# Optimization experiments

Hardware: AMD Instinct MI355X
Metric: run time of the kernel (lower is better)

Reference implementation:

```python
import jax, jax.numpy as jnp
import numpy as np

EMBED_DIM = 1024
NUM_HEADS = 16
NUM_GROUPS = 4
HEAD_DIM = EMBED_DIM // NUM_HEADS          # 64
KV_REPEAT = NUM_HEADS // NUM_GROUPS        # 4
KV_DIM = HEAD_DIM * NUM_GROUPS             # 256


def setup_inputs() -> dict:
    key = jax.random.key(0)
    ks = jax.random.split(key, 9)
    s = 0.02
    x = jax.random.normal(ks[0], (4, 2048, EMBED_DIM), dtype=jnp.float32)
    Wq = jax.random.normal(ks[1], (EMBED_DIM, EMBED_DIM), dtype=jnp.float32) * s
    bq = jnp.zeros((EMBED_DIM,), dtype=jnp.float32)
    Wk = jax.random.normal(ks[2], (EMBED_DIM, KV_DIM), dtype=jnp.float32) * s
    bk = jnp.zeros((KV_DIM,), dtype=jnp.float32)
    Wv = jax.random.normal(ks[3], (EMBED_DIM, KV_DIM), dtype=jnp.float32) * s
    bv = jnp.zeros((KV_DIM,), dtype=jnp.float32)
    Wo = jax.random.normal(ks[4], (EMBED_DIM, EMBED_DIM), dtype=jnp.float32) * s
    bo = jnp.zeros((EMBED_DIM,), dtype=jnp.float32)
    return {"x": x, "Wq": Wq, "bq": bq, "Wk": Wk, "bk": bk,
            "Wv": Wv, "bv": bv, "Wo": Wo, "bo": bo}


def reference(x, Wq, bq, Wk, bk, Wv, bv, Wo, bo):
    B, S, E = x.shape
    G, R, D = NUM_GROUPS, KV_REPEAT, HEAD_DIM
    scale = 1.0 / jnp.sqrt(jnp.float32(D))
    # projections
    q = (x @ Wq + bq).reshape(B, S, G, R, D)   # query head h = g*R + r, matching
    k = (x @ Wk + bk).reshape(B, S, G, D)      # torch repeat_interleave grouping
    v = (x @ Wv + bv).reshape(B, S, G, D)
    # scaled scores: [B, G, R, Sq, Sk] -- same O(n^2) math, no KV duplication
    scores = jnp.einsum('bqgrd,bkgd->bgrqk', q * scale, k)
    attn = jax.nn.softmax(scores, axis=-1)
    out = jnp.einsum('bgrqk,bkgd->bqgrd', attn, v).reshape(B, S, E)
    return out @ Wo + bo
```

## Files before the change

kernel.cpp:

```cpp
#include <hip/hip_runtime.h>
#include <hip/hip_bf16.h>
#include <cstdint>


#define B_  4
#define S_  2048
#define E_  1024
#define H_  16
#define G_  4
#define R_  4
#define D_  64
#define KV_ 256

typedef unsigned short u16;
typedef unsigned int u32;
typedef __attribute__((ext_vector_type(8))) __bf16 bf16x8;
typedef __attribute__((ext_vector_type(4))) float f32x4;

#if __has_builtin(__builtin_amdgcn_exp2f)
#define EXP2(x) __builtin_amdgcn_exp2f(x)
#else
#define EXP2(x) exp2f(x)
#endif

__device__ __forceinline__ float b2f(u16 v) {
    unsigned u = ((unsigned)v) << 16;
    return __builtin_bit_cast(float, u);
}
__device__ __forceinline__ u16 f2b(float f) {
    unsigned u = __builtin_bit_cast(unsigned, f);
    u += 0x7fffu + ((u >> 16) & 1u);
    return (u16)(u >> 16);
}
__device__ __forceinline__ u16 f2b_rtz(float f) {
    return (u16)(__builtin_bit_cast(unsigned, f) >> 16);
}

__device__ __forceinline__ int sniff_f32(const u16* w, int t) {
    bool hit = (w[t & 63] & 0x4000) != 0;
    return (__popcll(__ballot(hit)) > 4) ? 1 : 0;
}

__device__ __forceinline__ void gl_lds16(const u16* g, u16* l) {
    __builtin_amdgcn_global_load_lds(
        (const __attribute__((address_space(1))) u32*)(const void*)g,
        (__attribute__((address_space(3))) u32*)(void*)l, 16, 0, 0);
}

__global__ __launch_bounds__(256) void prep_all(
    const void* __restrict__ x,
    const void* __restrict__ Wq, const void* __restrict__ Wk,
    const void* __restrict__ Wv, const void* __restrict__ Wo,
    u16* __restrict__ xc, u16* __restrict__ WqT, u16* __restrict__ WkT,
    u16* __restrict__ WvT, u16* __restrict__ WoT)
{
    __shared__ u16 tile[64][65];
    const int f = sniff_f32((const u16*)Wq, threadIdx.x);
    int b = blockIdx.x;
    if (b < 4096) {
        int i0 = (b * 256 + threadIdx.x) * 8;
        if (f) {
            const float4* s = (const float4*)x;
            float4 a = s[i0 / 4], c = s[i0 / 4 + 1];
            uint4 o;
            o.x = (u32)f2b(a.x) | ((u32)f2b(a.y) << 16);
            o.y = (u32)f2b(a.z) | ((u32)f2b(a.w) << 16);
            o.z = (u32)f2b(c.x) | ((u32)f2b(c.y) << 16);
            o.w = (u32)f2b(c.z) | ((u32)f2b(c.w) << 16);
            *(uint4*)(xc + i0) = o;
        } else {
            *(uint4*)(xc + i0) = ((const uint4*)x)[i0 / 8];
        }
        return;
    }
    int j = b - 4096;
    const void* src; u16* dst; int N, nt, kt;
    if (j < 256)      {           src = Wq; dst = WqT; N = 1024; nt = j & 15; kt = j >> 4; }
    else if (j < 320) { j -= 256; src = Wk; dst = WkT; N = 256;  nt = j & 3;  kt = j >> 2; }
    else if (j < 384) { j -= 320; src = Wv; dst = WvT; N = 256;  nt = j & 3;  kt = j >> 2; }
    else              { j -= 384; src = Wo; dst = WoT; N = 1024; nt = j & 15; kt = j >> 4; }
    const int K = 1024;
    const int n0 = nt * 64, k0 = kt * 64;
    const int tr = threadIdx.x >> 6, tc = threadIdx.x & 63;
#pragma unroll
    for (int i = 0; i < 16; i++) {
        int k = k0 + i * 4 + tr;
        size_t idx = (size_t)k * N + n0 + tc;
        float v = f ? ((const float*)src)[idx] : b2f(((const u16*)src)[idx]);
        tile[i * 4 + tr][tc] = f2b(v);
    }
    __syncthreads();
#pragma unroll
    for (int i = 0; i < 16; i++) {
        int n = n0 + i * 4 + tr;
        dst[(size_t)n * K + k0 + tc] = tile[tc][i * 4 + tr];
    }
}

__device__ __forceinline__ float load_bias(const void* b, int i, int f) {
    return f ? ((const float*)b)[i] : b2f(((const u16*)b)[i]);
}

__global__ __launch_bounds__(256) void gemm_bt(
    const u16* __restrict__ A, const u16* __restrict__ Bt,
    const void* __restrict__ bA, const void* __restrict__ bB,
    const void* __restrict__ bC,
    void* __restrict__ Cv, void* __restrict__ Cv2, void* __restrict__ Cv3,
    int M, int N, int K, int mode, const u16* __restrict__ sniffw)
{
    __shared__ __align__(16) u16 As[128][64];
    __shared__ __align__(16) u16 Bs[128][64];

    const int t    = threadIdx.x;
    const int wave = t >> 6, lane = t & 63;
    const int lr   = lane & 15, quad = lane >> 4;
    const int kgrp = quad * 8;
    const int m0 = blockIdx.y * 128, n0 = blockIdx.x * 128;
    const int wm = (wave >> 1) * 64, wn = (wave & 1) * 64;
    const int f = sniff_f32(sniffw, t);

    f32x4 acc[4][4];
#pragma unroll
    for (int i = 0; i < 4; i++)
#pragma unroll
        for (int j = 0; j < 4; j++) acc[i][j] = (f32x4){0.f, 0.f, 0.f, 0.f};

    for (int k0 = 0; k0 < K; k0 += 64) {
#pragma unroll
        for (int i = 0; i < 4; i++) {
            int c = t + i * 256;
            int row = c >> 3, cc = (c & 7) * 8;
            int lbase = (i * 256 + wave * 64) * 8;
            gl_lds16(A  + (size_t)(m0 + row) * K + k0 + cc, &As[0][0] + lbase);
            gl_lds16(Bt + (size_t)(n0 + row) * K + k0 + cc, &Bs[0][0] + lbase);
        }
        __syncthreads();
#pragma unroll
        for (int s2 = 0; s2 < 2; ++s2) {
            bf16x8 af[4], bfr[4];
#pragma unroll
            for (int tm = 0; tm < 4; tm++)
                af[tm] = *(const bf16x8*)&As[wm + tm * 16 + lr][s2 * 32 + kgrp];
#pragma unroll
            for (int tn = 0; tn < 4; tn++)
                bfr[tn] = *(const bf16x8*)&Bs[wn + tn * 16 + lr][s2 * 32 + kgrp];
#pragma unroll
            for (int tm = 0; tm < 4; tm++)
#pragma unroll
                for (int tn = 0; tn < 4; tn++)
                    acc[tm][tn] = __builtin_amdgcn_mfma_f32_16x16x32_bf16(
                        af[tm], bfr[tn], acc[tm][tn], 0, 0, 0);
        }
        __syncthreads();
    }

#pragma unroll
    for (int tm = 0; tm < 4; tm++) {
        int rowb = m0 + wm + tm * 16 + quad * 4;
#pragma unroll
        for (int tn = 0; tn < 4; tn++) {
            int col = n0 + wn + tn * 16 + lr;
            float bv;
            if (mode == 2)           bv = load_bias(bA, col, f);
            else if (col < 1024)     bv = load_bias(bA, col, f);
            else if (col < 1280)     bv = load_bias(bB, col - 1024, f);
            else                     bv = load_bias(bC, col - 1280, f);
            if (mode == 4 && col >= 1280) {
                int c2 = col - 1280, g = c2 >> 6, d = c2 & 63;
                int bi = rowb >> 11, s = rowb & 2047;
                u16 h[4];
#pragma unroll
                for (int r = 0; r < 4; r++) h[r] = f2b(acc[tm][tn][r] + bv);
                uint2 pk;
                pk.x = (u32)h[0] | ((u32)h[1] << 16);
                pk.y = (u32)h[2] | ((u32)h[3] << 16);
                *(uint2*)&((u16*)Cv3)[((size_t)(bi * G_ + g) * D_ + d) * S_ + s] = pk;
                continue;
            }
#pragma unroll
            for (int r = 0; r < 4; r++) {
                int row = rowb + r;
                float val = acc[tm][tn][r] + bv;
                if (mode == 2) {
                    if (f) ((float*)Cv)[(size_t)row * N + col] = val;
                    else   ((u16*)Cv)[(size_t)row * N + col] = f2b(val);
                } else if (col < 1024) {
                    ((u16*)Cv)[(size_t)row * 1024 + col] = f2b(val * 0.18033688f);
                } else {
                    ((u16*)Cv2)[(size_t)row * 256 + (col - 1024)] = f2b(val);
                }
            }
        }
    }
}

__global__ __launch_bounds__(256) void flash_gqa(
    const u16* __restrict__ Q, const u16* __restrict__ Kb,
    const u16* __restrict__ Vt, u16* __restrict__ AO)
{
    __shared__ __align__(16) u16 Ks[64][72];
    __shared__ __align__(16) u16 Vs[64][72];
    __shared__ __align__(16) u16 Ps[4][64][40];

    const int t    = threadIdx.x;
    const int wave = t >> 6, lane = t & 63;
    const int lr   = lane & 15, quad = lane >> 4, kgrp = quad * 8;

    const int bg = blockIdx.x;
    const int bi = bg / G_, g = bg % G_;
    const int h  = g * R_ + wave;
    const int sq0 = blockIdx.y * 64;

    const u16* qp   = Q  + ((size_t)bi * S_ + sq0) * E_ + h * D_;
    const u16* kptr = Kb + (size_t)bi * S_ * KV_ + g * D_;
    const u16* vptr = Vt + (size_t)(bi * G_ + g) * D_ * S_;
    u16 (*Pw)[40] = Ps[wave];

    bf16x8 aq[4][2];
#pragma unroll
    for (int tm = 0; tm < 4; tm++)
#pragma unroll
        for (int s2 = 0; s2 < 2; s2++)
            aq[tm][s2] = *(const bf16x8*)(qp + (size_t)(tm * 16 + lr) * E_ + s2 * 32 + kgrp);

    float rs[16];
    f32x4 o[4][4];
#pragma unroll
    for (int i = 0; i < 16; i++) rs[i] = 0.f;
#pragma unroll
    for (int i = 0; i < 4; i++)
#pragma unroll
        for (int j = 0; j < 4; j++) o[i][j] = (f32x4){0.f, 0.f, 0.f, 0.f};

    for (int j = 0; j < S_ / 64; j++) {
        __syncthreads();
        int kb = j * 64;
#pragma unroll
        for (int i = 0; i < 2; i++) {
            int c = t + i * 256;
            int row = c >> 3, cc = (c & 7) * 8;
            *(uint4*)&Ks[row][cc] = *(const uint4*)(kptr + (size_t)(kb + row) * KV_ + cc);
            *(uint4*)&Vs[row][cc] = *(const uint4*)(vptr + (size_t)row * S_ + kb + cc);
        }
        __syncthreads();

#pragma unroll
        for (int h2 = 0; h2 < 2; h2++) {
#pragma unroll
            for (int tn2 = 0; tn2 < 2; tn2++) {
                int tn = h2 * 2 + tn2;
                f32x4 scc[4];
#pragma unroll
                for (int a = 0; a < 4; a++) scc[a] = (f32x4){0.f, 0.f, 0.f, 0.f};
#pragma unroll
                for (int s2 = 0; s2 < 2; ++s2) {
                    bf16x8 bk = *(const bf16x8*)&Ks[tn * 16 + lr][s2 * 32 + kgrp];
#pragma unroll
                    for (int tm = 0; tm < 4; tm++)
                        scc[tm] = __builtin_amdgcn_mfma_f32_16x16x32_bf16(
                            aq[tm][s2], bk, scc[tm], 0, 0, 0);
                }
#pragma unroll
                for (int tm = 0; tm < 4; tm++)
#pragma unroll
                    for (int r = 0; r < 4; r++) {
                        float p = EXP2(scc[tm][r]);
                        Pw[tm * 16 + quad * 4 + r][tn2 * 16 + lr] = f2b_rtz(p);
                        rs[tm * 4 + r] += p;
                    }
            }
            bf16x8 ap[4], bv[4];
#pragma unroll
            for (int tm = 0; tm < 4; tm++)
                ap[tm] = *(const bf16x8*)&Pw[tm * 16 + lr][kgrp];
#pragma unroll
            for (int td = 0; td < 4; td++)
                bv[td] = *(const bf16x8*)&Vs[td * 16 + lr][h2 * 32 + kgrp];
#pragma unroll
            for (int tm = 0; tm < 4; tm++)
#pragma unroll
                for (int td = 0; td < 4; td++)
                    o[tm][td] = __builtin_amdgcn_mfma_f32_16x16x32_bf16(
                        ap[tm], bv[td], o[tm][td], 0, 0, 0);
        }
    }

#pragma unroll
    for (int msk = 1; msk < 16; msk <<= 1)
#pragma unroll
        for (int i = 0; i < 16; i++) rs[i] += __shfl_xor(rs[i], msk);

#pragma unroll
    for (int tm = 0; tm < 4; tm++)
#pragma unroll
        for (int r = 0; r < 4; r++) {
            int s = sq0 + tm * 16 + quad * 4 + r;
            float inv = 1.0f / fmaxf(rs[tm * 4 + r], 1e-30f);
#pragma unroll
            for (int td = 0; td < 4; td++) {
                int d = td * 16 + lr;
                AO[(((size_t)bi * S_ + s) * H_ + h) * D_ + d] = f2b(o[tm][td][r] * inv);
            }
        }
}

extern "C" void kernel_launch(void* const* d_in, const int* in_sizes, int n_in,
                              void* d_out, int out_size, void* d_ws, size_t ws_size,
                              hipStream_t stream) {
    const void* x  = d_in[0];
    const void* Wq = d_in[1];
    const void* bq = d_in[2];
    const void* Wk = d_in[3];
    const void* bk = d_in[4];
    const void* Wv = d_in[5];
    const void* bv = d_in[6];
    const void* Wo = d_in[7];
    const void* bo = d_in[8];

    u16* ws  = (u16*)d_ws;
    u16* xc  = ws;
    u16* WqT = xc  + (size_t)8388608;
    u16* WkT = WqT + 1048576;
    u16* WvT = WkT + 262144;
    u16* WoT = WvT + 262144;
    u16* Qb  = WoT + 1048576;
    u16* Kb  = Qb  + (size_t)8388608;
    u16* Vtb = Kb  + (size_t)2097152;
    u16* AO  = Vtb + (size_t)2097152;

    size_t need = 2ull * ((size_t)(AO - ws) + 8388608ull);
    if (ws_size < need) return;

    prep_all<<<4736, 256, 0, stream>>>(x, Wq, Wk, Wv, Wo,
                                       xc, WqT, WkT, WvT, WoT);

    dim3 blk(256);
    gemm_bt<<<dim3(1536 / 128, 8192 / 128), blk, 0, stream>>>(
        xc, WqT, bq, bk, bv, Qb, Kb, Vtb, 8192, 1536, 1024, 4, (const u16*)Wq);
    flash_gqa<<<dim3(B_ * G_, S_ / 64), blk, 0, stream>>>(Qb, Kb, Vtb, AO);
    gemm_bt<<<dim3(1024 / 128, 8192 / 128), blk, 0, stream>>>(
        AO, WoT, bo, nullptr, nullptr, d_out, nullptr, nullptr,
        8192, 1024, 1024, 2, (const u16*)Wq);
}
```

Before: 326.6 us.

## Split flash attention block into 8 waves of 32 query rows with MFMA priority

```diff
diff --git a/kernel.cpp b/kernel.cpp
--- a/kernel.cpp
+++ b/kernel.cpp
@@ -194,13 +194,13 @@
     }
 }
 
-__global__ __launch_bounds__(256) void flash_gqa(
+__global__ __launch_bounds__(512, 4) void flash_gqa(
     const u16* __restrict__ Q, const u16* __restrict__ Kb,
     const u16* __restrict__ Vt, u16* __restrict__ AO)
 {
     __shared__ __align__(16) u16 Ks[64][72];
     __shared__ __align__(16) u16 Vs[64][72];
-    __shared__ __align__(16) u16 Ps[4][64][40];
+    __shared__ __align__(16) u16 Ps[8][32][40];
 
     const int t    = threadIdx.x;
     const int wave = t >> 6, lane = t & 63;
@@ -208,40 +208,39 @@
 
     const int bg = blockIdx.x;
     const int bi = bg / G_, g = bg % G_;
-    const int h  = g * R_ + wave;
-    const int sq0 = blockIdx.y * 64;
+    const int h  = g * R_ + (wave & 3);
+    const int sq0 = blockIdx.y * 64 + (wave >> 2) * 32;
 
     const u16* qp   = Q  + ((size_t)bi * S_ + sq0) * E_ + h * D_;
     const u16* kptr = Kb + (size_t)bi * S_ * KV_ + g * D_;
     const u16* vptr = Vt + (size_t)(bi * G_ + g) * D_ * S_;
     u16 (*Pw)[40] = Ps[wave];
 
-    bf16x8 aq[4][2];
-#pragma unroll
-    for (int tm = 0; tm < 4; tm++)
+    bf16x8 aq[2][2];
+#pragma unroll
+    for (int tm = 0; tm < 2; tm++)
 #pragma unroll
         for (int s2 = 0; s2 < 2; s2++)
             aq[tm][s2] = *(const bf16x8*)(qp + (size_t)(tm * 16 + lr) * E_ + s2 * 32 + kgrp);
 
-    float rs[16];
-    f32x4 o[4][4];
-#pragma unroll
-    for (int i = 0; i < 16; i++) rs[i] = 0.f;
-#pragma unroll
-    for (int i = 0; i < 4; i++)
+    float rs[8];
+    f32x4 o[2][4];
+#pragma unroll
+    for (int i = 0; i < 8; i++) rs[i] = 0.f;
+#pragma unroll
+    for (int i = 0; i < 2; i++)
 #pragma unroll
         for (int j = 0; j < 4; j++) o[i][j] = (f32x4){0.f, 0.f, 0.f, 0.f};
+
+    const int srow = t >> 3, scol = (t & 7) * 8;
+    const u16* kg = kptr + (size_t)srow * KV_ + scol;
+    const u16* vg = vptr + (size_t)srow * S_ + scol;
 
     for (int j = 0; j < S_ / 64; j++) {
         __syncthreads();
         int kb = j * 64;
-#pragma unroll
-        for (int i = 0; i < 2; i++) {
-            int c = t + i * 256;
-            int row = c >> 3, cc = (c & 7) * 8;
-            *(uint4*)&Ks[row][cc] = *(const uint4*)(kptr + (size_t)(kb + row) * KV_ + cc);
-            *(uint4*)&Vs[row][cc] = *(const uint4*)(vptr + (size_t)row * S_ + kb + cc);
-        }
+        *(uint4*)&Ks[srow][scol] = *(const uint4*)(kg + (size_t)kb * KV_);
+        *(uint4*)&Vs[srow][scol] = *(const uint4*)(vg + kb);
         __syncthreads();
 
 #pragma unroll
@@ -249,49 +248,53 @@
 #pragma unroll
             for (int tn2 = 0; tn2 < 2; tn2++) {
                 int tn = h2 * 2 + tn2;
-                f32x4 scc[4];
-#pragma unroll
-                for (int a = 0; a < 4; a++) scc[a] = (f32x4){0.f, 0.f, 0.f, 0.f};
+                f32x4 sc[2];
+#pragma unroll
+                for (int a = 0; a < 2; a++) sc[a] = (f32x4){0.f, 0.f, 0.f, 0.f};
+                __builtin_amdgcn_s_setprio(1);
 #pragma unroll
                 for (int s2 = 0; s2 < 2; ++s2) {
                     bf16x8 bk = *(const bf16x8*)&Ks[tn * 16 + lr][s2 * 32 + kgrp];
 #pragma unroll
-                    for (int tm = 0; tm < 4; tm++)
-                        scc[tm] = __builtin_amdgcn_mfma_f32_16x16x32_bf16(
-                            aq[tm][s2], bk, scc[tm], 0, 0, 0);
+                    for (int tm = 0; tm < 2; tm++)
+                        sc[tm] = __builtin_amdgcn_mfma_f32_16x16x32_bf16(
+                            aq[tm][s2], bk, sc[tm], 0, 0, 0);
                 }
-#pragma unroll
-                for (int tm = 0; tm < 4; tm++)
+                __builtin_amdgcn_s_setprio(0);
+#pragma unroll
+                for (int tm = 0; tm < 2; tm++)
 #pragma unroll
                     for (int r = 0; r < 4; r++) {
-                        float p = EXP2(scc[tm][r]);
+                        float p = EXP2(sc[tm][r]);
                         Pw[tm * 16 + quad * 4 + r][tn2 * 16 + lr] = f2b_rtz(p);
                         rs[tm * 4 + r] += p;
                     }
             }
-            bf16x8 ap[4], bv[4];
-#pragma unroll
-            for (int tm = 0; tm < 4; tm++)
+            bf16x8 ap[2], bv[4];
+#pragma unroll
+            for (int tm = 0; tm < 2; tm++)
                 ap[tm] = *(const bf16x8*)&Pw[tm * 16 + lr][kgrp];
 #pragma unroll
             for (int td = 0; td < 4; td++)
                 bv[td] = *(const bf16x8*)&Vs[td * 16 + lr][h2 * 32 + kgrp];
-#pragma unroll
-            for (int tm = 0; tm < 4; tm++)
+            __builtin_amdgcn_s_setprio(1);
+#pragma unroll
+            for (int tm = 0; tm < 2; tm++)
 #pragma unroll
                 for (int td = 0; td < 4; td++)
                     o[tm][td] = __builtin_amdgcn_mfma_f32_16x16x32_bf16(
                         ap[tm], bv[td], o[tm][td], 0, 0, 0);
+            __builtin_amdgcn_s_setprio(0);
         }
     }
 
 #pragma unroll
     for (int msk = 1; msk < 16; msk <<= 1)
 #pragma unroll
-        for (int i = 0; i < 16; i++) rs[i] += __shfl_xor(rs[i], msk);
-
-#pragma unroll
-    for (int tm = 0; tm < 4; tm++)
+        for (int i = 0; i < 8; i++) rs[i] += __shfl_xor(rs[i], msk);
+
+#pragma unroll
+    for (int tm = 0; tm < 2; tm++)
 #pragma unroll
         for (int r = 0; r < 4; r++) {
             int s = sq0 + tm * 16 + quad * 4 + r;
@@ -337,7 +340,7 @@
     dim3 blk(256);
     gemm_bt<<<dim3(1536 / 128, 8192 / 128), blk, 0, stream>>>(
         xc, WqT, bq, bk, bv, Qb, Kb, Vtb, 8192, 1536, 1024, 4, (const u16*)Wq);
-    flash_gqa<<<dim3(B_ * G_, S_ / 64), blk, 0, stream>>>(Qb, Kb, Vtb, AO);
+    flash_gqa<<<dim3(B_ * G_, S_ / 64), dim3(512), 0, stream>>>(Qb, Kb, Vtb, AO);
     gemm_bt<<<dim3(1024 / 128, 8192 / 128), blk, 0, stream>>>(
         AO, WoT, bo, nullptr, nullptr, d_out, nullptr, nullptr,
         8192, 1024, 1024, 2, (const u16*)Wq);
```

Measured after the change: 282.3 us. 13.5% less time.
